# Kernel optimization log

Hardware: AMD Instinct MI355X
Metric: run time of the kernel (lower is better)

The kernel has to match this reference:

```python
import jax, jax.numpy as jnp
import numpy as np

Cl, Nl, Cv, Nv, M = 32, 128, 8, 64, 500000


def _sample1d(line, g):
    # line: [C, N]; g in [-1,1]; align_corners=True, zeros padding
    C, N = line.shape
    ix = (g + 1.0) * 0.5 * (N - 1)
    i0 = jnp.floor(ix)
    w = ix - i0
    i0 = i0.astype(jnp.int32)
    def gth(i, wt):
        valid = (i >= 0) & (i < N)
        return line[:, jnp.clip(i, 0, N - 1)] * (wt * valid)
    return (gth(i0, 1.0 - w) + gth(i0 + 1, w)).T  # [M, C]


def _sample2d(plane, gx, gy):
    # plane: [C, H, W]; grid x -> W axis, y -> H axis (torch grid_sample convention)
    C, H, W = plane.shape
    ix = (gx + 1.0) * 0.5 * (W - 1)
    iy = (gy + 1.0) * 0.5 * (H - 1)
    x0 = jnp.floor(ix); y0 = jnp.floor(iy)
    wx = ix - x0; wy = iy - y0
    x0 = x0.astype(jnp.int32); y0 = y0.astype(jnp.int32)
    flat = plane.reshape(C, -1)
    def gth(xi, yi, wt):
        valid = (xi >= 0) & (xi < W) & (yi >= 0) & (yi < H)
        idx = jnp.clip(yi, 0, H - 1) * W + jnp.clip(xi, 0, W - 1)
        return flat[:, idx] * (wt * valid)
    out = (gth(x0, y0, (1 - wx) * (1 - wy)) + gth(x0 + 1, y0, wx * (1 - wy))
           + gth(x0, y0 + 1, (1 - wx) * wy) + gth(x0 + 1, y0 + 1, wx * wy))
    return out.T  # [M, C]


def _sample3d(vol, gx, gy, gz):
    # vol: [C, D, H, W]; grid (x,y,z) -> (W,H,D) axes
    C, D, H, W = vol.shape
    ix = (gx + 1.0) * 0.5 * (W - 1)
    iy = (gy + 1.0) * 0.5 * (H - 1)
    iz = (gz + 1.0) * 0.5 * (D - 1)
    x0 = jnp.floor(ix); y0 = jnp.floor(iy); z0 = jnp.floor(iz)
    wx = ix - x0; wy = iy - y0; wz = iz - z0
    x0 = x0.astype(jnp.int32); y0 = y0.astype(jnp.int32); z0 = z0.astype(jnp.int32)
    flat = vol.reshape(C, -1)
    out = 0.0
    for dz in (0, 1):
        for dy in (0, 1):
            for dx in (0, 1):
                xi, yi, zi = x0 + dx, y0 + dy, z0 + dz
                wt = ((wx if dx else 1 - wx) * (wy if dy else 1 - wy) * (wz if dz else 1 - wz))
                valid = (xi >= 0) & (xi < W) & (yi >= 0) & (yi < H) & (zi >= 0) & (zi < D)
                idx = (jnp.clip(zi, 0, D - 1) * H + jnp.clip(yi, 0, H - 1)) * W + jnp.clip(xi, 0, W - 1)
                out = out + flat[:, idx] * (wt * valid)
    return out.T  # [M, C]


def setup_inputs() -> dict:
    key = jax.random.key(0)
    ks = jax.random.split(key, 16)
    rng, shift = 0.4, 0.1
    coordinates = jax.random.uniform(ks[0], (1, M, 3), minval=-1.0, maxval=1.0)
    line_x = jax.random.uniform(ks[1], (Cl, Nl)) * rng + shift
    line_y = jax.random.uniform(ks[2], (Cl, Nl)) * rng + shift
    line_z = jax.random.uniform(ks[3], (Cl, Nl)) * rng + shift
    plane_xy = jax.random.normal(ks[4], (Cl, Nl, Nl)) * rng + shift
    plane_yz = jax.random.normal(ks[5], (Cl, Nl, Nl)) * rng + shift
    plane_xz = jax.random.normal(ks[6], (Cl, Nl, Nl)) * rng + shift
    volume = jax.random.normal(ks[7], (Cv, Nv, Nv, Nv)) * rng + shift
    def lin(k, fi, fo):
        k1, k2 = jax.random.split(k)
        lim = 1.0 / np.sqrt(fi)
        return (jax.random.uniform(k1, (fi, fo), minval=-lim, maxval=lim),
                jax.random.uniform(k2, (fo,), minval=-lim, maxval=lim))
    Wx, bx = lin(ks[8], Cl, Cl)
    Wy, by = lin(ks[9], Cl, Cl)
    Wz, bz = lin(ks[10], Cl, Cl)
    W1, b1 = lin(ks[11], Cl + Cv, 128)
    W2, b2 = lin(ks[12], 128, 1)
    return dict(coordinates=coordinates, line_x=line_x, line_y=line_y, line_z=line_z,
                plane_xy=plane_xy, plane_yz=plane_yz, plane_xz=plane_xz, volume=volume,
                Wx=Wx, bx=bx, Wy=Wy, by=by, Wz=Wz, bz=bz, W1=W1, b1=b1, W2=W2, b2=b2)


def reference(coordinates, line_x, line_y, line_z, plane_xy, plane_yz, plane_xz, volume,
              Wx, bx, Wy, by, Wz, bz, W1, b1, W2, b2):
    c = coordinates[0]  # [M, 3], batch squeezed like the torch code
    x, y, z = c[:, 0], c[:, 1], c[:, 2]
    x_e = _sample1d(line_x, x)
    y_e = _sample1d(line_y, y)
    z_e = _sample1d(line_z, z)
    xy_e = _sample2d(plane_xy, x, y)
    yz_e = _sample2d(plane_yz, y, z)
    xz_e = _sample2d(plane_xz, x, z)
    xyz_e = _sample3d(volume, x, y, z)
    phi = lambda e, W, b: jax.nn.relu(e) @ W + b  # Sequential(ReLU, Linear)
    yztran = phi(yz_e, Wx, bx)
    xztran = phi(xz_e, Wy, by)
    xytran = phi(xy_e, Wz, bz)
    xtran = phi(x_e, Wx, bx)
    ytran = phi(y_e, Wy, by)
    ztran = phi(z_e, Wz, bz)
    features = xtran * yztran + ytran * xztran + ztran * xytran
    features = jnp.concatenate([features, xyz_e], axis=-1)  # [M, Cl+Cv]
    h = jax.nn.relu(features @ W1 + b1)
    return h @ W2 + b2  # [M, 1]
```

## Files before the change

### kernel.cpp

```cpp
#include <hip/hip_runtime.h>

typedef unsigned short u16;
typedef u16 u16x8 __attribute__((ext_vector_type(8)));
typedef _Float16 half2 __attribute__((ext_vector_type(2)));
typedef _Float16 h8v __attribute__((ext_vector_type(8)));
typedef float f4v __attribute__((ext_vector_type(4)));
typedef unsigned int u32;
typedef u32 u32x4 __attribute__((ext_vector_type(4)));

union H8 { h8v v; half2 p[4]; };

static __device__ __forceinline__ float bf2f(u16 u) {
    union { unsigned int i; float f; } v;
    v.i = ((unsigned int)u) << 16;
    return v.f;
}
static __device__ __forceinline__ u16 f2bf(float f) {
    union { float f; unsigned int i; } v;
    v.f = f;
    unsigned int x = v.i;
    x += 0x7fffu + ((x >> 16) & 1u);
    return (u16)(x >> 16);
}
static __device__ __forceinline__ float gld(int dt, const void* p, int i) {
    return dt ? ((const float*)p)[i] : bf2f(((const u16*)p)[i]);
}
static __device__ __forceinline__ int detect_dt(const void* coords) {
    u16 v = ((const u16*)coords)[threadIdx.x & 63];
    int e = (v >> 7) & 0xFF;
    bool inr = (e >= 90) && (e <= 126);
    unsigned long long m = __ballot(inr);
    return (__popcll(m) >= 56) ? 0 : 1;
}
static __device__ __forceinline__ half2 pk(float a, float b) {
    return __builtin_bit_cast(half2, __builtin_amdgcn_cvt_pkrtz(a, b));
}

static __device__ __forceinline__ void lds_wait() {
    asm volatile("s_waitcnt lgkmcnt(0)" ::: "memory");
}

#define WF_OFF        64u
#define PLANES_S_OFF  34304u
#define VOL_S_OFF     3180032u
#define LINES_S_OFF   7374336u
#define PART_OFF      7398912u
#define TOT_OFF       9496064u
#define REC_OFF       9512448u

#define NBUCK 4096
#define HBLOCKS 256

static __device__ __forceinline__ int make_key3(float x, float y, float z) {
    int kx = min(max((int)((x + 1.0f) * 8.0f), 0), 15);
    int ky = min(max((int)((y + 1.0f) * 8.0f), 0), 15);
    int kz = min(max((int)((z + 1.0f) * 8.0f), 0), 15);
    return (kz * 16 + ky) * 16 + kx;
}
static __device__ __forceinline__ int make_key(int dt, const void* coords, int p) {
    return make_key3(gld(dt, coords, p * 3 + 0), gld(dt, coords, p * 3 + 1),
                     gld(dt, coords, p * 3 + 2));
}

static __device__ __forceinline__ void weights_work(
    int dt, int r,
    const void* Wx, const void* bx, const void* Wy, const void* by,
    const void* Wz, const void* bz, const void* W1, const void* b1,
    const void* W2, const void* b2, float* wbase)
{
    _Float16* WtH = (_Float16*)wbase;
    float*    bv  = wbase + 1536;
    _Float16* W1H = (_Float16*)(wbase + 1632);
    float*    b1v = wbase + 5728;
    float*    W2v = wbase + 5856;
    float*    b2v = wbase + 5984;
    if (r < 3072) {
        int m = r >> 10, idx = r & 1023;
        int o = idx >> 5, c = idx & 31;
        const void* s = (m == 0) ? Wx : (m == 1) ? Wy : Wz;
        WtH[r] = (_Float16)gld(dt, s, c * 32 + o);
    } else if (r < 3168) {
        int q2 = r - 3072;
        int m = q2 >> 5, c = q2 & 31;
        const void* s = (m == 0) ? bx : (m == 1) ? by : bz;
        bv[q2] = gld(dt, s, c);
    } else if (r < 11360) {
        int idx = r - 3168;
        int j = idx >> 6, i = idx & 63;
        W1H[idx] = (i < 40) ? (_Float16)gld(dt, W1, i * 128 + j) : (_Float16)0.0f;
    } else if (r < 11488) {
        b1v[r - 11360] = gld(dt, b1, r - 11360);
    } else if (r < 11616) {
        W2v[r - 11488] = gld(dt, W2, r - 11488);
    } else if (r == 11616) {
        b2v[0] = gld(dt, b2, 0);
    }
}

__global__ __launch_bounds__(256) void kp_prep_all(
    const void* __restrict__ coords,
    const void* __restrict__ lx, const void* __restrict__ ly,
    const void* __restrict__ lz,
    const void* __restrict__ pxy, const void* __restrict__ pyz,
    const void* __restrict__ pxz, const void* __restrict__ vol,
    const void* __restrict__ Wx, const void* __restrict__ bx,
    const void* __restrict__ Wy, const void* __restrict__ by,
    const void* __restrict__ Wz, const void* __restrict__ bz,
    const void* __restrict__ W1, const void* __restrict__ b1,
    const void* __restrict__ W2, const void* __restrict__ b2,
    float* __restrict__ wbase,
    u16* __restrict__ planes_s, u16* __restrict__ vol_s,
    u16* __restrict__ lines_s, u16* __restrict__ part, int M)
{
    __shared__ unsigned int lh[NBUCK];
    int dt = detect_dt(coords);
    int blk = blockIdx.x;
    if (blk < 1798) {
        int t = blk * 256 + threadIdx.x;
        u16x8 v;
        if (t < 196608) {
            int o = t * 8;
            int pl = o >> 19;
            int r  = o & 524287;
            int pos = r >> 5, c0 = r & 31;
            const void* src = (pl == 0) ? pxy : (pl == 1) ? pyz : pxz;
#pragma unroll
            for (int i = 0; i < 8; ++i)
                v[i] = dt ? f2bf(((const float*)src)[(c0 + i) * 16384 + pos])
                          : ((const u16*)src)[(c0 + i) * 16384 + pos];
            *(u16x8*)(planes_s + o) = v;
        } else if (t < 458752) {
            int pos = t - 196608;
#pragma unroll
            for (int c = 0; c < 8; ++c)
                v[c] = dt ? f2bf(((const float*)vol)[c * 262144 + pos])
                          : ((const u16*)vol)[c * 262144 + pos];
            *(u16x8*)(vol_s + pos * 8) = v;
        } else {
            int o = (t - 458752) * 8;
            int l = o >> 12, rr = o & 4095;
            int pos = rr >> 5, c0 = rr & 31;
            const void* src = (l == 0) ? lx : (l == 1) ? ly : lz;
#pragma unroll
            for (int i = 0; i < 8; ++i)
                v[i] = dt ? f2bf(((const float*)src)[(c0 + i) * 128 + pos])
                          : ((const u16*)src)[(c0 + i) * 128 + pos];
            *(u16x8*)(lines_s + o) = v;
        }
    } else if (blk < 1844) {
        int r = (blk - 1798) * 256 + threadIdx.x;
        weights_work(dt, r, Wx, bx, Wy, by, Wz, bz, W1, b1, W2, b2, wbase);
    } else {
        int b = blk - 1844;
        for (int i = threadIdx.x; i < NBUCK; i += 256) lh[i] = 0u;
        __syncthreads();
        for (int p = b * 256 + threadIdx.x; p < M; p += HBLOCKS * 256)
            atomicAdd(&lh[make_key(dt, coords, p)], 1u);
        __syncthreads();
        for (int i = threadIdx.x; i < NBUCK; i += 256)
            part[b * NBUCK + i] = (u16)lh[i];
    }
}

__global__ __launch_bounds__(256) void kp_colscan(
    u16* __restrict__ part, unsigned int* __restrict__ tot)
{
    int lane = threadIdx.x & 63;
    int bkt  = blockIdx.x * 4 + (threadIdx.x >> 6);
    unsigned int v[4];
    unsigned int ltot = 0;
#pragma unroll
    for (int i = 0; i < 4; ++i) {
        v[i] = part[(lane * 4 + i) * NBUCK + bkt];
        ltot += v[i];
    }
    unsigned int x = ltot;
#pragma unroll
    for (int d = 1; d < 64; d <<= 1) {
        unsigned int y = __shfl_up(x, d);
        if (lane >= d) x += y;
    }
    unsigned int run = x - ltot;
#pragma unroll
    for (int i = 0; i < 4; ++i) {
        part[(lane * 4 + i) * NBUCK + bkt] = (u16)run;
        run += v[i];
    }
    if (lane == 63) tot[bkt] = x;
}

__global__ __launch_bounds__(256) void kp_scatter_det(
    const void* __restrict__ coords, const u16* __restrict__ part,
    const unsigned int* __restrict__ tot,
    u32* __restrict__ recs, int M)
{
    __shared__ unsigned int cnt[NBUCK];
    __shared__ unsigned int psum[256];
    int b = blockIdx.x;
    int t = threadIdx.x;
    unsigned int bs[16];
    unsigned int s = 0;
#pragma unroll
    for (int i = 0; i < 16; ++i) {
        bs[i] = tot[t * 16 + i];
        s += bs[i];
    }
    psum[t] = s;
    __syncthreads();
#pragma unroll
    for (int d = 1; d < 256; d <<= 1) {
        unsigned int v = (t >= d) ? psum[t - d] : 0u;
        __syncthreads();
        psum[t] += v;
        __syncthreads();
    }
    unsigned int run = psum[t] - s;
#pragma unroll
    for (int i = 0; i < 16; ++i) {
        int bkt = t * 16 + i;
        cnt[bkt] = run + (unsigned int)part[b * NBUCK + bkt];
        run += bs[i];
    }
    __syncthreads();
    int dt = detect_dt(coords);
    const u16* cu = (const u16*)coords;
    for (int p = b * 256 + t; p < M; p += HBLOCKS * 256) {
        float x = gld(dt, coords, p * 3 + 0);
        float y = gld(dt, coords, p * 3 + 1);
        float z = gld(dt, coords, p * 3 + 2);
        int key = make_key3(x, y, z);
        unsigned int pos = atomicAdd(&cnt[key], 1u);
        u32x4 r;
        r.x = (u32)p;
        if (dt == 0) {
            r.y = (u32)cu[p * 3 + 0] | ((u32)cu[p * 3 + 1] << 16);
            r.z = (u32)cu[p * 3 + 2];
        } else {
            r.y = 0u; r.z = 0u;
        }
        r.w = 0u;
        *(u32x4*)(recs + (size_t)pos * 4u) = r;
    }
}

struct Samp { int i0, i1; float w0, w1; };

static __device__ __forceinline__ Samp make_samp(float g, int N) {
    float ix = (g + 1.0f) * 0.5f * (float)(N - 1);
    float fl = floorf(ix);
    float w  = ix - fl;
    int i  = (int)fl;
    int i1 = i + 1;
    float v0 = (i  >= 0 && i  < N) ? 1.0f : 0.0f;
    float v1 = (i1 >= 0 && i1 < N) ? 1.0f : 0.0f;
    Samp s;
    s.w0 = (1.0f - w) * v0;
    s.w1 = w * v1;
    s.i0 = min(max(i, 0), N - 1);
    s.i1 = min(max(i1, 0), N - 1);
    return s;
}

#define MFMA16(a, b, c) __builtin_amdgcn_mfma_f32_16x16x32_f16((a), (b), (c), 0, 0, 0)

#define SRE 40
#define SR2 72

struct PL { u16x8 q00[4], q01[4], q10[4], q11[4]; };
struct VL { u16x8 v[8]; };

static __device__ __forceinline__ void plane_load(
    const u16* __restrict__ Ps, const Samp& sa, const Samp& sb, PL& P)
{
    const u16x8* p00 = (const u16x8*)(Ps + (sb.i0 * 128 + sa.i0) * 32);
    const u16x8* p01 = (const u16x8*)(Ps + (sb.i0 * 128 + sa.i1) * 32);
    const u16x8* p10 = (const u16x8*)(Ps + (sb.i1 * 128 + sa.i0) * 32);
    const u16x8* p11 = (const u16x8*)(Ps + (sb.i1 * 128 + sa.i1) * 32);
#pragma unroll
    for (int cc = 0; cc < 4; ++cc) {
        P.q00[cc] = p00[cc]; P.q01[cc] = p01[cc];
        P.q10[cc] = p10[cc]; P.q11[cc] = p11[cc];
    }
}

static __device__ __forceinline__ void vol_loads(
    const u16* __restrict__ vol_s, const Samp& vx, const Samp& vy,
    const Samp& vz, VL& V)
{
#pragma unroll
    for (int corner = 0; corner < 8; ++corner) {
        int dx = corner & 1, dy = (corner >> 1) & 1, dz = corner >> 2;
        int xi = dx ? vx.i1 : vx.i0;
        int yi = dy ? vy.i1 : vy.i0;
        int zi = dz ? vz.i1 : vz.i0;
        V.v[corner] = *(const u16x8*)(vol_s + (((zi * 64) + yi) * 64 + xi) * 8);
    }
}

template<int PRE>
static __device__ __forceinline__ void term_step(
    int lane, int q, int l15,
    const u16* __restrict__ Ls, const Samp& sl,
    const PL& P, const Samp& sa, const Samp& sb,
    const _Float16* __restrict__ Wt, const float* __restrict__ bvt,
    _Float16* El, _Float16* Ep, float (&feat)[4][2][4],
    const u16* __restrict__ nps, const Samp& na, const Samp& nb, PL& PN,
    const u16* __restrict__ vol_s, const Samp& vx, const Samp& vy,
    const Samp& vz, VL& V)
{
    const u16x8* l0 = (const u16x8*)(Ls + sl.i0 * 32);
    const u16x8* l1 = (const u16x8*)(Ls + sl.i1 * 32);
    float w00 = sb.w0 * sa.w0, w01 = sb.w0 * sa.w1;
    float w10 = sb.w1 * sa.w0, w11 = sb.w1 * sa.w1;
#pragma unroll
    for (int cc = 0; cc < 4; ++cc) {
        u16x8 A0 = l0[cc], A1 = l1[cc];
        u16x8 Q00 = P.q00[cc], Q01 = P.q01[cc];
        u16x8 Q10 = P.q10[cc], Q11 = P.q11[cc];
        H8 hl, hp;
#pragma unroll
        for (int kk = 0; kk < 4; ++kk) {
            int k0 = 2 * kk, k1 = k0 + 1;
            float el0 = sl.w0 * bf2f(A0[k0]) + sl.w1 * bf2f(A1[k0]);
            float el1 = sl.w0 * bf2f(A0[k1]) + sl.w1 * bf2f(A1[k1]);
            float ep0 = w00 * bf2f(Q00[k0]) + w01 * bf2f(Q01[k0])
                      + w10 * bf2f(Q10[k0]) + w11 * bf2f(Q11[k0]);
            float ep1 = w00 * bf2f(Q00[k1]) + w01 * bf2f(Q01[k1])
                      + w10 * bf2f(Q10[k1]) + w11 * bf2f(Q11[k1]);
            hl.p[kk] = pk(fmaxf(el0, 0.0f), fmaxf(el1, 0.0f));
            hp.p[kk] = pk(fmaxf(ep0, 0.0f), fmaxf(ep1, 0.0f));
        }
        *(h8v*)&El[lane * SRE + cc * 8] = hl.v;
        *(h8v*)&Ep[lane * SRE + cc * 8] = hp.v;
    }
    if constexpr (PRE == 1) plane_load(nps, na, nb, PN);
    if constexpr (PRE == 2) vol_loads(vol_s, vx, vy, vz, V);

    h8v bf0 = *(const h8v*)&Wt[(l15) * 32 + q * 8];
    h8v bf1 = *(const h8v*)&Wt[(16 + l15) * 32 + q * 8];
    float bb0 = bvt[l15], bb1 = bvt[16 + l15];
    f4v c0 = {bb0, bb0, bb0, bb0};
    f4v c1 = {bb1, bb1, bb1, bb1};
    lds_wait();
#pragma unroll
    for (int mt = 0; mt < 4; ++mt) {
        h8v aL = *(const h8v*)&El[(mt * 16 + l15) * SRE + q * 8];
        h8v aP = *(const h8v*)&Ep[(mt * 16 + l15) * SRE + q * 8];
        f4v ta0 = MFMA16(aL, bf0, c0);
        f4v tb0 = MFMA16(aP, bf0, c0);
        f4v ta1 = MFMA16(aL, bf1, c1);
        f4v tb1 = MFMA16(aP, bf1, c1);
#pragma unroll
        for (int r = 0; r < 4; ++r) {
            feat[mt][0][r] += ta0[r] * tb0[r];
            feat[mt][1][r] += ta1[r] * tb1[r];
        }
    }
    lds_wait();
}

__global__ __launch_bounds__(64) void kp_main_mfma(
    const void* __restrict__ coords, const u32* __restrict__ recs,
    const u16* __restrict__ planes_s, const u16* __restrict__ vol_s,
    const u16* __restrict__ lines_s,
    const float* __restrict__ wbase,
    void* __restrict__ out, int M)
{
    __shared__ _Float16 eb[5120];
    __shared__ float res[64];
    int dt = detect_dt(coords);
    const _Float16* WtH = (const _Float16*)wbase;
    const float*    bv  = wbase + 1536;
    const _Float16* W1H = (const _Float16*)(wbase + 1632);
    const float*    b1v = wbase + 5728;
    const float*    W2v = wbase + 5856;
    const float*    b2v = wbase + 5984;

    int lane = threadIdx.x;
    int q = lane >> 4, l15 = lane & 15;
    _Float16* El = eb;
    _Float16* Ep = eb + 2560;
    _Float16* E2 = eb;

    int p = blockIdx.x * 64 + lane;
    p = min(p, M - 1);
    u32x4 rv = *(const u32x4*)(recs + (size_t)p * 4u);
    int sp = (int)rv.x;

    float x, y, z;
    if (dt == 0) {
        x = bf2f((u16)(rv.y & 0xffffu));
        y = bf2f((u16)(rv.y >> 16));
        z = bf2f((u16)(rv.z & 0xffffu));
    } else {
        x = ((const float*)coords)[sp * 3 + 0];
        y = ((const float*)coords)[sp * 3 + 1];
        z = ((const float*)coords)[sp * 3 + 2];
    }

    Samp sx = make_samp(x, 128), sy = make_samp(y, 128), sz = make_samp(z, 128);

    float feat[4][2][4];
#pragma unroll
    for (int mt = 0; mt < 4; ++mt)
#pragma unroll
        for (int n = 0; n < 2; ++n)
#pragma unroll
            for (int r = 0; r < 4; ++r) feat[mt][n][r] = 0.0f;

    PL Pa, Pb;
    VL V;
    Samp vx, vy, vz;

    plane_load(planes_s + 1 * 524288, sy, sz, Pa);

    term_step<1>(lane, q, l15, lines_s + 0 * 4096, sx, Pa, sy, sz,
                 WtH + 0, bv + 0, El, Ep, feat,
                 planes_s + 2 * 524288, sx, sz, Pb,
                 vol_s, sx, sx, sx, V);

    term_step<1>(lane, q, l15, lines_s + 1 * 4096, sy, Pb, sx, sz,
                 WtH + 1024, bv + 32, El, Ep, feat,
                 planes_s + 0 * 524288, sx, sy, Pa,
                 vol_s, sx, sx, sx, V);

    vx = make_samp(x, 64); vy = make_samp(y, 64); vz = make_samp(z, 64);

    term_step<2>(lane, q, l15, lines_s + 2 * 4096, sz, Pa, sx, sy,
                 WtH + 2048, bv + 64, El, Ep, feat,
                 planes_s, sx, sy, Pb,
                 vol_s, vx, vy, vz, V);

#pragma unroll
    for (int mt = 0; mt < 4; ++mt)
#pragma unroll
        for (int n = 0; n < 2; ++n)
#pragma unroll
            for (int r = 0; r < 4; ++r)
                E2[(mt * 16 + q * 4 + r) * SR2 + n * 16 + l15] =
                    (_Float16)feat[mt][n][r];
    {
        float vf[8];
#pragma unroll
        for (int c = 0; c < 8; ++c) vf[c] = 0.0f;
#pragma unroll
        for (int corner = 0; corner < 8; ++corner) {
            int dx = corner & 1, dy = (corner >> 1) & 1, dz = corner >> 2;
            float w = (dx ? vx.w1 : vx.w0) * (dy ? vy.w1 : vy.w0)
                    * (dz ? vz.w1 : vz.w0);
            u16x8 v = V.v[corner];
#pragma unroll
            for (int c = 0; c < 8; ++c)
                vf[c] = fmaf(w, bf2f(v[c]), vf[c]);
        }
        H8 hv;
#pragma unroll
        for (int k = 0; k < 4; ++k) hv.p[k] = pk(vf[2 * k], vf[2 * k + 1]);
        *(h8v*)&E2[lane * SR2 + 32] = hv.v;
        h8v zz = {};
        *(h8v*)&E2[lane * SR2 + 40] = zz;
        *(h8v*)&E2[lane * SR2 + 48] = zz;
        *(h8v*)&E2[lane * SR2 + 56] = zz;
    }
    lds_wait();

    h8v af[4][2];
#pragma unroll
    for (int mt = 0; mt < 4; ++mt)
#pragma unroll
        for (int ks = 0; ks < 2; ++ks)
            af[mt][ks] = *(const h8v*)&E2[(mt * 16 + l15) * SR2 + ks * 32 + q * 8];

    float s[4][4];
#pragma unroll
    for (int mt = 0; mt < 4; ++mt)
#pragma unroll
        for (int r = 0; r < 4; ++r) s[mt][r] = 0.0f;

#pragma unroll
    for (int NT = 0; NT < 8; ++NT) {
        int o = NT * 16 + l15;
        h8v b0  = *(const h8v*)&W1H[o * 64 + q * 8];
        h8v b1f = *(const h8v*)&W1H[o * 64 + 32 + q * 8];
        float w2 = W2v[o];
        float bb = b1v[o];
        f4v cinit = {bb, bb, bb, bb};
#pragma unroll
        for (int mt = 0; mt < 4; ++mt) {
            f4v c = MFMA16(af[mt][0], b0, cinit);
            c = MFMA16(af[mt][1], b1f, c);
#pragma unroll
            for (int r = 0; r < 4; ++r)
                s[mt][r] = fmaf(fmaxf(c[r], 0.0f), w2, s[mt][r]);
        }
    }
#pragma unroll
    for (int mt = 0; mt < 4; ++mt)
#pragma unroll
        for (int r = 0; r < 4; ++r) {
            float v = s[mt][r];
            v += __shfl_xor(v, 1);
            v += __shfl_xor(v, 2);
            v += __shfl_xor(v, 4);
            v += __shfl_xor(v, 8);
            s[mt][r] = v;
        }
    if (l15 == 0) {
#pragma unroll
        for (int mt = 0; mt < 4; ++mt)
#pragma unroll
            for (int r = 0; r < 4; ++r)
                res[mt * 16 + q * 4 + r] = s[mt][r];
    }
    lds_wait();
    float rr = res[lane] + b2v[0];
    if (dt) ((float*)out)[sp] = rr;
    else    ((u16*)out)[sp] = f2bf(rr);
}

__global__ void kp_prep_weights_fb(
    const void* __restrict__ coords,
    const void* __restrict__ Wx, const void* __restrict__ bx,
    const void* __restrict__ Wy, const void* __restrict__ by,
    const void* __restrict__ Wz, const void* __restrict__ bz,
    const void* __restrict__ W1, const void* __restrict__ b1,
    const void* __restrict__ W2, const void* __restrict__ b2,
    float* __restrict__ wbase)
{
    int dt = detect_dt(coords);
    int t = blockIdx.x * blockDim.x + threadIdx.x;
    weights_work(dt, t, Wx, bx, Wy, by, Wz, bz, W1, b1, W2, b2, wbase);
}

__global__ __launch_bounds__(256) void kp_main_direct(
    const void* __restrict__ coords,
    const void* __restrict__ lx, const void* __restrict__ ly, const void* __restrict__ lz,
    const void* __restrict__ pxy, const void* __restrict__ pyz, const void* __restrict__ pxz,
    const void* __restrict__ vol,
    const float* __restrict__ wbase,
    void* __restrict__ out, int M)
{
    int dt = detect_dt(coords);
    const _Float16* WtH = (const _Float16*)wbase;
    const float*    bv  = wbase + 1536;
    const _Float16* W1H = (const _Float16*)(wbase + 1632);
    const float*    b1v = wbase + 5728;
    const float*    W2v = wbase + 5856;
    const float*    b2v = wbase + 5984;

    int p = blockIdx.x * 256 + threadIdx.x;
    p = min(p, M - 1);

    float x = gld(dt, coords, p * 3 + 0);
    float y = gld(dt, coords, p * 3 + 1);
    float z = gld(dt, coords, p * 3 + 2);

    Samp sx = make_samp(x, 128), sy = make_samp(y, 128), sz = make_samp(z, 128);

    float feat[40];
#pragma unroll
    for (int o = 0; o < 40; ++o) feat[o] = 0.0f;

    const void* Ls[3] = {lx, ly, lz};
    const void* Psv[3] = {pyz, pxz, pxy};
    Samp sl3[3] = {sx, sy, sz};
    Samp sa3[3] = {sy, sx, sx};
    Samp sb3[3] = {sz, sz, sy};
#pragma unroll 1
    for (int m = 0; m < 3; ++m) {
        float ta[32], tb[32];
        const float* bvt = bv + m * 32;
        const _Float16* Wt = WtH + m * 1024;
#pragma unroll
        for (int o = 0; o < 32; ++o) { ta[o] = bvt[o]; tb[o] = bvt[o]; }
        Samp sl = sl3[m], sa = sa3[m], sb = sb3[m];
        float w00 = sb.w0 * sa.w0, w01 = sb.w0 * sa.w1;
        float w10 = sb.w1 * sa.w0, w11 = sb.w1 * sa.w1;
        int i00 = sb.i0 * 128 + sa.i0, i01 = sb.i0 * 128 + sa.i1;
        int i10 = sb.i1 * 128 + sa.i0, i11 = sb.i1 * 128 + sa.i1;
#pragma unroll 1
        for (int c = 0; c < 32; ++c) {
            float el = sl.w0 * gld(dt, Ls[m], c * 128 + sl.i0)
                     + sl.w1 * gld(dt, Ls[m], c * 128 + sl.i1);
            float ep = w00 * gld(dt, Psv[m], c * 16384 + i00)
                     + w01 * gld(dt, Psv[m], c * 16384 + i01)
                     + w10 * gld(dt, Psv[m], c * 16384 + i10)
                     + w11 * gld(dt, Psv[m], c * 16384 + i11);
            float r1 = fmaxf(el, 0.0f), r2 = fmaxf(ep, 0.0f);
#pragma unroll
            for (int o = 0; o < 32; ++o) {
                float w = (float)Wt[o * 32 + c];
                ta[o] = fmaf(r1, w, ta[o]);
                tb[o] = fmaf(r2, w, tb[o]);
            }
        }
#pragma unroll
        for (int o = 0; o < 32; ++o) feat[o] = fmaf(ta[o], tb[o], feat[o]);
    }

    Samp vx = make_samp(x, 64), vy = make_samp(y, 64), vz = make_samp(z, 64);
#pragma unroll 1
    for (int corner = 0; corner < 8; ++corner) {
        int dx = corner & 1, dy = (corner >> 1) & 1, dz = corner >> 2;
        int xi = dx ? vx.i1 : vx.i0;
        int yi = dy ? vy.i1 : vy.i0;
        int zi = dz ? vz.i1 : vz.i0;
        float w = (dx ? vx.w1 : vx.w0) * (dy ? vy.w1 : vy.w0) * (dz ? vz.w1 : vz.w0);
        int pos = ((zi * 64) + yi) * 64 + xi;
#pragma unroll
        for (int c = 0; c < 8; ++c)
            feat[32 + c] = fmaf(w, gld(dt, vol, c * 262144 + pos), feat[32 + c]);
    }

    float acc_out = b2v[0];
#pragma unroll 2
    for (int j = 0; j < 128; ++j) {
        float acc = b1v[j];
        const _Float16* wr = W1H + j * 64;
#pragma unroll
        for (int i = 0; i < 40; ++i)
            acc = fmaf(feat[i], (float)wr[i], acc);
        acc_out = fmaf(fmaxf(acc, 0.0f), W2v[j], acc_out);
    }
    if (dt) ((float*)out)[p] = acc_out;
    else    ((u16*)out)[p] = f2bf(acc_out);
}

extern "C" void kernel_launch(void* const* d_in, const int* in_sizes, int n_in,
                              void* d_out, int out_size, void* d_ws, size_t ws_size,
                              hipStream_t stream) {
    const void* coords = d_in[0];
    const void* lx  = d_in[1];
    const void* ly  = d_in[2];
    const void* lz  = d_in[3];
    const void* pxy = d_in[4];
    const void* pyz = d_in[5];
    const void* pxz = d_in[6];
    const void* vol = d_in[7];
    const void* Wx  = d_in[8];
    const void* bx  = d_in[9];
    const void* Wy  = d_in[10];
    const void* by  = d_in[11];
    const void* Wz  = d_in[12];
    const void* bz  = d_in[13];
    const void* W1  = d_in[14];
    const void* b1  = d_in[15];
    const void* W2  = d_in[16];
    const void* b2  = d_in[17];

    int M = in_sizes[0] / 3;

    char* ws = (char*)d_ws;
    float*        wbase    = (float*)(ws + WF_OFF);
    u16*          planes_s = (u16*)(ws + PLANES_S_OFF);
    u16*          vol_s    = (u16*)(ws + VOL_S_OFF);
    u16*          lines_s  = (u16*)(ws + LINES_S_OFF);
    u16*          part     = (u16*)(ws + PART_OFF);
    unsigned int* tot      = (unsigned int*)(ws + TOT_OFF);
    u32*          recs     = (u32*)(ws + REC_OFF);

    size_t need_sorted = (size_t)REC_OFF + (size_t)M * 16u;

    if (ws_size >= need_sorted) {
        kp_prep_all<<<2100, 256, 0, stream>>>(coords, lx, ly, lz, pxy, pyz, pxz, vol,
                                              Wx, bx, Wy, by, Wz, bz, W1, b1, W2, b2,
                                              wbase, planes_s, vol_s, lines_s, part, M);
        kp_colscan<<<NBUCK / 4, 256, 0, stream>>>(part, tot);
        kp_scatter_det<<<HBLOCKS, 256, 0, stream>>>(coords, part, tot, recs, M);
        int blocks64 = (M + 63) / 64;
        kp_main_mfma<<<blocks64, 64, 0, stream>>>(coords, recs,
                                                  planes_s, vol_s, lines_s,
                                                  wbase, d_out, M);
    } else {
        int blocks = (M + 255) / 256;
        kp_prep_weights_fb<<<46, 256, 0, stream>>>(coords, Wx, bx, Wy, by, Wz, bz,
                                                   W1, b1, W2, b2, wbase);
        kp_main_direct<<<blocks, 256, 0, stream>>>(coords, lx, ly, lz, pxy, pyz, pxz,
                                                   vol, wbase, d_out, M);
    }
}
```

Measured before the change: 202.1 us.

## Fuse column scan and scatter into one cooperative kernel with grid sync

Merges the per-bucket column scan and the deterministic scatter into a single cooperative launch, separated by a grid-wide barrier. This removes one kernel launch and its inter-kernel gap. Each of the HBLOCKS blocks scans 16 buckets before the barrier. If the cooperative launch fails, it falls back to the original two kernels. The grid sync adds its own barrier cost and needs all blocks to be co-resident.

```diff
diff --git a/kernel.cpp b/kernel.cpp
--- a/kernel.cpp
+++ b/kernel.cpp
@@ -1,4 +1,5 @@
 #include <hip/hip_runtime.h>
+#include <hip/hip_cooperative_groups.h>
 
 typedef unsigned short u16;
 typedef u16 u16x8 __attribute__((ext_vector_type(8)));
@@ -162,7 +163,91 @@
     }
 }
 
-__global__ __launch_bounds__(256) void kp_colscan(
+__global__ __launch_bounds__(256) void kp_scan_scatter(
+    const void* __restrict__ coords, u16* __restrict__ part,
+    unsigned int* __restrict__ tot,
+    u32* __restrict__ recs, int M)
+{
+    __shared__ unsigned int cnt[NBUCK];
+    __shared__ unsigned int psum[256];
+    int b = blockIdx.x;
+    int t = threadIdx.x;
+    int lane = t & 63;
+    int wv   = t >> 6;
+
+#pragma unroll 1
+    for (int ib = 0; ib < 4; ++ib) {
+        int bkt = b * 16 + wv * 4 + ib;
+        unsigned int v[4];
+        unsigned int ltot = 0;
+#pragma unroll
+        for (int i = 0; i < 4; ++i) {
+            v[i] = part[(lane * 4 + i) * NBUCK + bkt];
+            ltot += v[i];
+        }
+        unsigned int x = ltot;
+#pragma unroll
+        for (int d = 1; d < 64; d <<= 1) {
+            unsigned int y = __shfl_up(x, d);
+            if (lane >= d) x += y;
+        }
+        unsigned int run = x - ltot;
+#pragma unroll
+        for (int i = 0; i < 4; ++i) {
+            part[(lane * 4 + i) * NBUCK + bkt] = (u16)run;
+            run += v[i];
+        }
+        if (lane == 63) tot[bkt] = x;
+    }
+    __threadfence();
+    cooperative_groups::this_grid().sync();
+
+    unsigned int bs[16];
+    unsigned int s = 0;
+#pragma unroll
+    for (int i = 0; i < 16; ++i) {
+        bs[i] = tot[t * 16 + i];
+        s += bs[i];
+    }
+    psum[t] = s;
+    __syncthreads();
+#pragma unroll
+    for (int d = 1; d < 256; d <<= 1) {
+        unsigned int v = (t >= d) ? psum[t - d] : 0u;
+        __syncthreads();
+        psum[t] += v;
+        __syncthreads();
+    }
+    unsigned int run = psum[t] - s;
+#pragma unroll
+    for (int i = 0; i < 16; ++i) {
+        int bkt = t * 16 + i;
+        cnt[bkt] = run + (unsigned int)part[b * NBUCK + bkt];
+        run += bs[i];
+    }
+    __syncthreads();
+    int dt = detect_dt(coords);
+    const u16* cu = (const u16*)coords;
+    for (int p = b * 256 + t; p < M; p += HBLOCKS * 256) {
+        float x = gld(dt, coords, p * 3 + 0);
+        float y = gld(dt, coords, p * 3 + 1);
+        float z = gld(dt, coords, p * 3 + 2);
+        int key = make_key3(x, y, z);
+        unsigned int pos = atomicAdd(&cnt[key], 1u);
+        u32x4 r;
+        r.x = (u32)p;
+        if (dt == 0) {
+            r.y = (u32)cu[p * 3 + 0] | ((u32)cu[p * 3 + 1] << 16);
+            r.z = (u32)cu[p * 3 + 2];
+        } else {
+            r.y = 0u; r.z = 0u;
+        }
+        r.w = 0u;
+        *(u32x4*)(recs + (size_t)pos * 4u) = r;
+    }
+}
+
+__global__ __launch_bounds__(256) void kp_colscan_fb(
     u16* __restrict__ part, unsigned int* __restrict__ tot)
 {
     int lane = threadIdx.x & 63;
@@ -189,7 +274,7 @@
     if (lane == 63) tot[bkt] = x;
 }
 
-__global__ __launch_bounds__(256) void kp_scatter_det(
+__global__ __launch_bounds__(256) void kp_scatter_fb(
     const void* __restrict__ coords, const u16* __restrict__ part,
     const unsigned int* __restrict__ tot,
     u32* __restrict__ recs, int M)
@@ -665,8 +750,19 @@
         kp_prep_all<<<2100, 256, 0, stream>>>(coords, lx, ly, lz, pxy, pyz, pxz, vol,
                                               Wx, bx, Wy, by, Wz, bz, W1, b1, W2, b2,
                                               wbase, planes_s, vol_s, lines_s, part, M);
-        kp_colscan<<<NBUCK / 4, 256, 0, stream>>>(part, tot);
-        kp_scatter_det<<<HBLOCKS, 256, 0, stream>>>(coords, part, tot, recs, M);
+        {
+            void* cvd = (void*)coords;
+            void* args[] = {(void*)&cvd, (void*)&part, (void*)&tot,
+                            (void*)&recs, (void*)&M};
+            hipError_t e = hipLaunchCooperativeKernel(
+                (const void*)kp_scan_scatter, dim3(HBLOCKS), dim3(256),
+                args, 0, stream);
+            if (e != hipSuccess) {
+                kp_colscan_fb<<<NBUCK / 4, 256, 0, stream>>>(part, tot);
+                kp_scatter_fb<<<HBLOCKS, 256, 0, stream>>>(coords, part, tot,
+                                                           recs, M);
+            }
+        }
         int blocks64 = (M + 63) / 64;
         kp_main_mfma<<<blocks64, 64, 0, stream>>>(coords, recs,
                                                   planes_s, vol_s, lines_s,
```

Result: slower. 312.0 us (+54.4%).
